# Kernel optimization log

Measured on AMD Instinct MI355X. Metric: run time of the kernel, lower is better.

The kernel has to match this reference:

```python
import jax, jax.numpy as jnp
import numpy as np

# Constants (mirroring CONSTANTS.py choices)
BCL = 8          # BYTE_CONTEXT_LEN
BED = 32         # BYTE_EMBED_DIM
HID = 512        # CONVERSATIONAL_HIDDEN_DIM
VOCAB = 260      # BYTE_VOCAB_DIM
NULL = 256
SOS = 257
B, T = 64, 512
NUMD = 16
CTX_DIM = HID + (50 + 64 + 150) + NUMD  # 792
IN_DIM = CTX_DIM + BCL * BED            # 1048


def setup_inputs() -> dict:
    key = jax.random.key(0)
    ks = jax.random.split(key, 20)
    s = 0.05
    return {
        "embedded_conversation_context": jax.random.normal(ks[0], (B, HID), jnp.float32),
        "next_packet_categorical": jax.random.randint(ks[1], (B, 3), 0, 10),
        "next_packet_numerical": jax.random.normal(ks[2], (B, NUMD), jnp.float32),
        "target_payload": jax.random.randint(ks[3], (B, T), 0, 256),
        "cat_emb_0": jax.random.normal(ks[4], (10, 50), jnp.float32) * s,
        "cat_emb_1": jax.random.normal(ks[5], (128, 64), jnp.float32) * s,
        "cat_emb_2": jax.random.normal(ks[6], (300, 150), jnp.float32) * s,
        "byte_emb": jax.random.normal(ks[7], (VOCAB, BED), jnp.float32) * s,
        "W_ih0": jax.random.normal(ks[8], (4 * HID, IN_DIM), jnp.float32) * s,
        "W_hh0": jax.random.normal(ks[9], (4 * HID, HID), jnp.float32) * s,
        "b_ih0": jax.random.normal(ks[10], (4 * HID,), jnp.float32) * s,
        "b_hh0": jax.random.normal(ks[11], (4 * HID,), jnp.float32) * s,
        "W_ih1": jax.random.normal(ks[12], (4 * HID, HID), jnp.float32) * s,
        "W_hh1": jax.random.normal(ks[13], (4 * HID, HID), jnp.float32) * s,
        "b_ih1": jax.random.normal(ks[14], (4 * HID,), jnp.float32) * s,
        "b_hh1": jax.random.normal(ks[15], (4 * HID,), jnp.float32) * s,
        "W_out": jax.random.normal(ks[16], (VOCAB - 4, HID), jnp.float32) * s,
        "b_out": jax.random.normal(ks[17], (VOCAB - 4,), jnp.float32) * s,
    }


def _lstm_layer(x, W_ih, W_hh, b_ih, b_hh):
    # x: [B, T, D] -> outputs [B, T, H]; torch gate order i, f, g, o
    xt = jnp.swapaxes(x, 0, 1)  # [T, B, D]
    gx = jnp.einsum('tbd,gd->tbg', xt, W_ih) + b_ih  # precompute input gates
    h0 = jnp.zeros((x.shape[0], HID), x.dtype)
    c0 = jnp.zeros((x.shape[0], HID), x.dtype)

    def step(carry, g_in):
        h, c = carry
        g = g_in + h @ W_hh.T + b_hh
        i, f, gg, o = jnp.split(g, 4, axis=-1)
        c = jax.nn.sigmoid(f) * c + jax.nn.sigmoid(i) * jnp.tanh(gg)
        h = jax.nn.sigmoid(o) * jnp.tanh(c)
        return (h, c), h

    _, ys = jax.lax.scan(step, (h0, c0), gx)
    return jnp.swapaxes(ys, 0, 1)  # [B, T, H]


def reference(embedded_conversation_context, next_packet_categorical,
              next_packet_numerical, target_payload,
              cat_emb_0, cat_emb_1, cat_emb_2, byte_emb,
              W_ih0, W_hh0, b_ih0, b_hh0,
              W_ih1, W_hh1, b_ih1, b_hh1,
              W_out, b_out):
    # categorical embeddings + context concat
    cat = jnp.concatenate([
        cat_emb_0[next_packet_categorical[:, 0]],
        cat_emb_1[next_packet_categorical[:, 1]],
        cat_emb_2[next_packet_categorical[:, 2]],
    ], axis=-1)
    context = jnp.concatenate([embedded_conversation_context, cat,
                               next_packet_numerical], axis=-1)  # [B, CTX_DIM]

    # front-pad payload with NULL*(BCL-1) then SOS, embed, sliding windows
    bsz = target_payload.shape[0]
    padded = jnp.concatenate([
        jnp.full((bsz, BCL - 1), NULL, target_payload.dtype),
        jnp.full((bsz, 1), SOS, target_payload.dtype),
        target_payload,
    ], axis=1)                                     # [B, T+BCL]
    emb = byte_emb[padded]                          # [B, T+BCL, BED]
    idx = jnp.arange(T)[:, None] + jnp.arange(BCL)[None, :]  # [T, BCL]
    win = emb[:, idx].reshape(bsz, T, BCL * BED)    # fused sliding-window gather

    ctx_rep = jnp.broadcast_to(context[:, None, :], (bsz, T, context.shape[-1]))
    x = jnp.concatenate([ctx_rep, win], axis=-1)    # [B, T, IN_DIM]

    h1 = _lstm_layer(x, W_ih0, W_hh0, b_ih0, b_hh0)
    h2 = _lstm_layer(h1, W_ih1, W_hh1, b_ih1, b_hh1)
    logits = jnp.einsum('bth,vh->btv', h2, W_out) + b_out  # [B, T, 256]
    return logits
```

## Files before the change

### kernel.cpp

```cpp
#include <hip/hip_runtime.h>
#include <hip/hip_bf16.h>
#include <math.h>

typedef __bf16 bf16;
typedef __bf16 bf16x8 __attribute__((ext_vector_type(8)));
typedef float  f32x4  __attribute__((ext_vector_type(4)));
typedef unsigned long long u64;

#define MFMA16(a, b, c) __builtin_amdgcn_mfma_f32_16x16x32_bf16((a), (b), (c), 0, 0, 0)

#define BB 64
#define TT 512
#define HH 512
#define G4 2048
#define NROW 32768
#define K2 1024
#define K3 1536
#define NWG 256
#define LROW 1032

#define AGLD(p) __hip_atomic_load((p), __ATOMIC_RELAXED, __HIP_MEMORY_SCOPE_AGENT)
#define AGST(p, v) __hip_atomic_store((p), (v), __ATOMIC_RELAXED, __HIP_MEMORY_SCOPE_AGENT)

__device__ __forceinline__ float sigmoidf_(float x) { return 1.0f / (1.0f + expf(-x)); }

__device__ __forceinline__ unsigned pack32(float h) {
    bf16 hh = (bf16)h;
    bf16 hl = (bf16)(h - (float)hh);
    unsigned short uh = __builtin_bit_cast(unsigned short, hh);
    unsigned short ul = __builtin_bit_cast(unsigned short, hl);
    return (unsigned)uh | ((unsigned)ul << 16);
}

__global__ void pad_bytes(const int* __restrict__ payload, int* __restrict__ bytes) {
    int b = blockIdx.x;
    for (int p = threadIdx.x; p < 520; p += blockDim.x)
        bytes[b * 520 + p] = (p < 7) ? 256 : ((p == 7) ? 257 : payload[b * 512 + p - 8]);
}

__global__ void build_Z(const float* __restrict__ Wih0, const float* __restrict__ bemb,
                        float* __restrict__ Z) {
    int v = blockIdx.x, j = blockIdx.y;
    __shared__ float e[32];
    if (threadIdx.x < 32) e[threadIdx.x] = bemb[v * 32 + threadIdx.x];
    __syncthreads();
#pragma unroll
    for (int i = 0; i < 8; i++) {
        int mp = threadIdx.x + i * 256;
        int u = mp >> 2, g = mp & 3;
        const float* wr = Wih0 + (size_t)(g * 512 + u) * 1048 + 792 + j * 32;
        float sum = 0.f;
#pragma unroll
        for (int kk = 0; kk < 32; kk++) sum += wr[kk] * e[kk];
        Z[((size_t)(v * 8 + j)) * G4 + mp] = sum;
    }
}

__global__ void build_ctxg(const float* __restrict__ ecc, const int* __restrict__ npc,
                           const float* __restrict__ npn,
                           const float* __restrict__ cat0, const float* __restrict__ cat1,
                           const float* __restrict__ cat2,
                           const float* __restrict__ bih0, const float* __restrict__ bhh0,
                           const float* __restrict__ Wih0, float* __restrict__ ctxg) {
    int b = blockIdx.x;
    __shared__ float cs[792];
    for (int k = threadIdx.x; k < 792; k += blockDim.x) {
        float v;
        if (k < 512)       v = ecc[b * 512 + k];
        else if (k < 562)  v = cat0[npc[b * 3 + 0] * 50 + (k - 512)];
        else if (k < 626)  v = cat1[npc[b * 3 + 1] * 64 + (k - 562)];
        else if (k < 776)  v = cat2[npc[b * 3 + 2] * 150 + (k - 626)];
        else               v = npn[b * 16 + (k - 776)];
        cs[k] = v;
    }
    __syncthreads();
#pragma unroll
    for (int i = 0; i < 8; i++) {
        int mp = threadIdx.x + i * 256;
        int u = mp >> 2, g = mp & 3;
        int orow = g * 512 + u;
        const float* wr = Wih0 + (size_t)orow * 1048;
        float sum = bih0[orow] + bhh0[orow];
        for (int k = 0; k < 792; k++) sum += wr[k] * cs[k];
        ctxg[b * G4 + mp] = sum;
    }
}

__global__ void conv_w0(const float* __restrict__ Whh0, bf16* __restrict__ W0p) {
    int rp = blockIdx.x; int u = rp >> 2, g = rp & 3;
    const float* src = Whh0 + (size_t)(g * 512 + u) * 512;
    bf16* dst = W0p + (size_t)rp * K2;
    for (int k = threadIdx.x; k < 512; k += blockDim.x) {
        float w = src[k]; bf16 hi = (bf16)w; bf16 lo = (bf16)(w - (float)hi);
        dst[k] = hi; dst[512 + k] = lo;
    }
}
__global__ void conv_w1(const float* __restrict__ Wih1, const float* __restrict__ Whh1,
                        bf16* __restrict__ W1p) {
    int rp = blockIdx.x; int u = rp >> 2, g = rp & 3;
    const float* s0 = Wih1 + (size_t)(g * 512 + u) * 512;
    const float* s1 = Whh1 + (size_t)(g * 512 + u) * 512;
    bf16* dst = W1p + (size_t)rp * (2 * K2);
    for (int k = threadIdx.x; k < 512; k += blockDim.x) {
        float w0 = s0[k]; bf16 h0 = (bf16)w0; bf16 l0 = (bf16)(w0 - (float)h0);
        dst[k] = h0; dst[512 + k] = l0;
        float w1 = s1[k]; bf16 h1 = (bf16)w1; bf16 l1 = (bf16)(w1 - (float)h1);
        dst[1024 + k] = h1; dst[1536 + k] = l1;
    }
}
__global__ void conv_wout(const float* __restrict__ Wout, bf16* __restrict__ Woutp) {
    int r = blockIdx.x;
    const float* src = Wout + (size_t)r * 512;
    bf16* dst = Woutp + (size_t)r * K3;
    for (int k = threadIdx.x; k < 512; k += blockDim.x) {
        float w = src[k]; bf16 hi = (bf16)w; bf16 lo = (bf16)(w - (float)hi);
        dst[k] = hi; dst[512 + k] = hi; dst[1024 + k] = lo;
    }
}
__global__ void conv_bias(const float* __restrict__ bih1, const float* __restrict__ bhh1,
                          float* __restrict__ bias1p) {
    int rp = blockIdx.x * blockDim.x + threadIdx.x;
    if (rp >= G4) return;
    int u = rp >> 2, g = rp & 3; int orow = g * 512 + u;
    bias1p[rp] = bih1[orow] + bhh1[orow];
}

__device__ __forceinline__ void group_barrier(unsigned* slots, int myslot, int bg,
                                              int tid, unsigned s1) {
    __syncthreads();
    __threadfence_block();
    if (tid == 0) AGST(&slots[myslot], s1);
    if (tid < 64) {
        int p = tid;
        int wpoll = (p < 32) ? (p * 4 + bg) : (128 + (p - 32) * 4 + bg);
        while (AGLD(&slots[wpoll]) < s1) __builtin_amdgcn_s_sleep(1);
    }
    __threadfence_block();
    __syncthreads();
}

__global__ __launch_bounds__(256, 1) void lstm_persist(
        const bf16* __restrict__ W0p, const bf16* __restrict__ W1p,
        const float* __restrict__ bias1p, const float* __restrict__ ctxg,
        const float* __restrict__ Z, const int* __restrict__ bytes,
        bf16* __restrict__ h0a, bf16* __restrict__ h0b,
        bf16* __restrict__ h1a, bf16* __restrict__ h1b,
        bf16* __restrict__ h2all, unsigned* __restrict__ slots) {
    __shared__ __align__(16) bf16 lds[2][16][LROW];
    int w = blockIdx.x, tid = threadIdx.x;
    int wave = tid >> 6, lane = tid & 63, l15 = lane & 15, q = lane >> 4;

    if (w < 128) {
        int mg = w >> 2, bg = w & 3;
        int b = bg * 16 + l15;
        int u = mg * 16 + wave * 4 + q;
        int u0 = mg * 16 + wave * 4;
        bf16x8 A[16][2];
        {
            const bf16* Ab = W0p + (size_t)(mg * 64 + wave * 16 + l15) * K2 + q * 8;
#pragma unroll
            for (int ks = 0; ks < 16; ks++) {
                A[ks][0] = *(const bf16x8*)(Ab + ks * 32);
                A[ks][1] = *(const bf16x8*)(Ab + 512 + ks * 32);
            }
        }
        f32x4 ctxgv = *(const f32x4*)&ctxg[b * G4 + 4 * u];
        const int* bp0 = bytes + b * 520;
        float c = 0.f;
        for (int s = 0; s <= TT; s++) {
            if (s < TT) {
                int t = s;
                const bf16* hr = (s & 1) ? h0a : h0b;
                const u64* g64 = (const u64*)(hr + (size_t)(bg * 16) * K2);
                u64 tmp[16];
#pragma unroll
                for (int i = 0; i < 8; i++) {
                    int cch = tid + i * 256;
                    tmp[2 * i]     = AGLD(&g64[2 * cch]);
                    tmp[2 * i + 1] = AGLD(&g64[2 * cch + 1]);
                }
                int vt[8];
#pragma unroll
                for (int j = 0; j < 8; j++) vt[j] = bp0[t + j];
                f32x4 g = ctxgv;
#pragma unroll
                for (int j = 0; j < 8; j++)
                    g += *(const f32x4*)&Z[((size_t)((vt[j] << 3) + j)) * G4 + 4 * u];
#pragma unroll
                for (int i = 0; i < 8; i++) {
                    int cch = tid + i * 256;
                    int br = cch >> 7, off = cch & 127;
                    u64 pr[2] = { tmp[2 * i], tmp[2 * i + 1] };
                    *(int4*)&lds[0][br][off * 8] = *(const int4*)pr;
                }
                __syncthreads();
                f32x4 a0 = {0.f,0.f,0.f,0.f}, a1 = a0, a2 = a0;
#pragma unroll
                for (int ks = 0; ks < 16; ks++) {
                    bf16x8 bhh = *(const bf16x8*)&lds[0][l15][ks * 32 + q * 8];
                    bf16x8 bhl = *(const bf16x8*)&lds[0][l15][512 + ks * 32 + q * 8];
                    a0 = MFMA16(A[ks][0], bhh, a0);
                    a1 = MFMA16(A[ks][0], bhl, a1);
                    a2 = MFMA16(A[ks][1], bhh, a2);
                }
                f32x4 acc = a0 + a1 + a2;
                float gi = acc[0] + g[0], gf = acc[1] + g[1], gg = acc[2] + g[2], go = acc[3] + g[3];
                float cnew = sigmoidf_(gf) * c + sigmoidf_(gi) * tanhf(gg);
                c = cnew;
                float h = sigmoidf_(go) * tanhf(cnew);
                unsigned hv = pack32(h);
                unsigned p0 = __shfl(hv, l15);
                unsigned p1 = __shfl(hv, l15 + 16);
                unsigned p2 = __shfl(hv, l15 + 32);
                unsigned p3 = __shfl(hv, l15 + 48);
                if (q == 0) {
                    u64 hhp = (u64)(p0 & 0xFFFFu) | ((u64)(p1 & 0xFFFFu) << 16)
                            | ((u64)(p2 & 0xFFFFu) << 32) | ((u64)(p3 & 0xFFFFu) << 48);
                    u64 hlp = (u64)(p0 >> 16) | ((u64)(p1 >> 16) << 16)
                            | ((u64)(p2 >> 16) << 32) | ((u64)(p3 >> 16) << 48);
                    bf16* hw = ((s & 1) ? h0b : h0a) + (size_t)b * K2;
                    AGST((u64*)&hw[u0], hhp);
                    AGST((u64*)&hw[512 + u0], hlp);
                }
            }
            if (s < TT) group_barrier(slots, w, bg, tid, (unsigned)(s + 1));
        }
    } else {
        int v = w - 128;
        int mg = v >> 2, bg = v & 3;
        int b = bg * 16 + l15;
        int u = mg * 16 + wave * 4 + q;
        int u0 = mg * 16 + wave * 4;
        bf16x8 A[2][16][2];
        {
            const bf16* Ab = W1p + (size_t)(mg * 64 + wave * 16 + l15) * (2 * K2) + q * 8;
#pragma unroll
            for (int m = 0; m < 2; m++)
#pragma unroll
                for (int ks = 0; ks < 16; ks++) {
                    A[m][ks][0] = *(const bf16x8*)(Ab + m * 1024 + ks * 32);
                    A[m][ks][1] = *(const bf16x8*)(Ab + m * 1024 + 512 + ks * 32);
                }
        }
        f32x4 bi = *(const f32x4*)&bias1p[4 * u];
        float c = 0.f;
        for (int s = 0; s <= TT; s++) {
            if (s >= 1) {
                int t = s - 1;
                const bf16* hr0 = (s & 1) ? h0a : h0b;
                const bf16* hr1 = (s & 1) ? h1a : h1b;
                const u64* g0 = (const u64*)(hr0 + (size_t)(bg * 16) * K2);
                const u64* g1 = (const u64*)(hr1 + (size_t)(bg * 16) * K2);
                u64 tmp[32];
#pragma unroll
                for (int i = 0; i < 8; i++) {
                    int cch = tid + i * 256;
                    tmp[2 * i]      = AGLD(&g0[2 * cch]);
                    tmp[2 * i + 1]  = AGLD(&g0[2 * cch + 1]);
                    tmp[16 + 2 * i] = AGLD(&g1[2 * cch]);
                    tmp[17 + 2 * i] = AGLD(&g1[2 * cch + 1]);
                }
#pragma unroll
                for (int i = 0; i < 8; i++) {
                    int cch = tid + i * 256;
                    int br = cch >> 7, off = cch & 127;
                    u64 p0_[2] = { tmp[2 * i], tmp[2 * i + 1] };
                    u64 p1_[2] = { tmp[16 + 2 * i], tmp[17 + 2 * i] };
                    *(int4*)&lds[0][br][off * 8] = *(const int4*)p0_;
                    *(int4*)&lds[1][br][off * 8] = *(const int4*)p1_;
                }
                __syncthreads();
                f32x4 a0 = {0.f,0.f,0.f,0.f}, a1 = a0, a2 = a0;
#pragma unroll
                for (int ks = 0; ks < 16; ks++) {
                    bf16x8 b0h = *(const bf16x8*)&lds[0][l15][ks * 32 + q * 8];
                    bf16x8 b0l = *(const bf16x8*)&lds[0][l15][512 + ks * 32 + q * 8];
                    a0 = MFMA16(A[0][ks][0], b0h, a0);
                    a1 = MFMA16(A[0][ks][0], b0l, a1);
                    a2 = MFMA16(A[0][ks][1], b0h, a2);
                    bf16x8 b1h = *(const bf16x8*)&lds[1][l15][ks * 32 + q * 8];
                    bf16x8 b1l = *(const bf16x8*)&lds[1][l15][512 + ks * 32 + q * 8];
                    a0 = MFMA16(A[1][ks][0], b1h, a0);
                    a1 = MFMA16(A[1][ks][0], b1l, a1);
                    a2 = MFMA16(A[1][ks][1], b1h, a2);
                }
                f32x4 acc = a0 + a1 + a2;
                float gi = acc[0] + bi[0], gf = acc[1] + bi[1], gg = acc[2] + bi[2], go = acc[3] + bi[3];
                float cnew = sigmoidf_(gf) * c + sigmoidf_(gi) * tanhf(gg);
                c = cnew;
                float h = sigmoidf_(go) * tanhf(cnew);
                unsigned hv = pack32(h);
                unsigned p0 = __shfl(hv, l15);
                unsigned p1 = __shfl(hv, l15 + 16);
                unsigned p2 = __shfl(hv, l15 + 32);
                unsigned p3 = __shfl(hv, l15 + 48);
                if (q == 0) {
                    u64 hhp = (u64)(p0 & 0xFFFFu) | ((u64)(p1 & 0xFFFFu) << 16)
                            | ((u64)(p2 & 0xFFFFu) << 32) | ((u64)(p3 & 0xFFFFu) << 48);
                    u64 hlp = (u64)(p0 >> 16) | ((u64)(p1 >> 16) << 16)
                            | ((u64)(p2 >> 16) << 32) | ((u64)(p3 >> 16) << 48);
                    bf16* hw = ((s & 1) ? h1b : h1a) + (size_t)b * K2;
                    AGST((u64*)&hw[u0], hhp);
                    AGST((u64*)&hw[512 + u0], hlp);
                    bf16* h2 = h2all + ((size_t)(t * 64 + b)) * K2;
                    *(u64*)&h2[u0] = hhp;
                    *(u64*)&h2[512 + u0] = hlp;
                }
            }
            if (s < TT) group_barrier(slots, w, bg, tid, (unsigned)(s + 1));
        }
    }
}

__global__ __launch_bounds__(256, 2) void gemm_out(const bf16* __restrict__ Wp,
                                                   const bf16* __restrict__ H2,
                                                   const float* __restrict__ bout,
                                                   float* __restrict__ out) {
    __shared__ bf16 As[128 * 32];
    __shared__ bf16 Bs[128 * 32];
    int mt = blockIdx.x, nt = blockIdx.y;
    int tid = threadIdx.x, wave = tid >> 6, lane = tid & 63;
    int l15 = lane & 15, q = lane >> 4;
    int msub = (wave & 1) * 64, nsub = (wave >> 1) * 64;
    f32x4 acc[4][4] = {};
    const bf16* Abase = Wp + (size_t)(mt * 128) * K3;
    const bf16* Bbase = H2 + (size_t)(nt * 128) * K2;
    for (int ks = 0; ks < K3 / 32; ks++) {
        int k0 = ks * 32;
        int kb = (k0 < 1024) ? k0 : (k0 - 1024);
        __syncthreads();
#pragma unroll
        for (int rnd = 0; rnd < 2; rnd++) {
            int cch = tid + rnd * 256;
            int rr = cch >> 2, seg = cch & 3;
            *(int4*)&As[cch * 8] = *(const int4*)&Abase[(size_t)rr * K3 + k0 + seg * 8];
            *(int4*)&Bs[cch * 8] = *(const int4*)&Bbase[(size_t)rr * K2 + kb + seg * 8];
        }
        __syncthreads();
        bf16x8 af[4], bf_[4];
#pragma unroll
        for (int i = 0; i < 4; i++) af[i]  = *(const bf16x8*)&As[(msub + i * 16 + l15) * 32 + q * 8];
#pragma unroll
        for (int j = 0; j < 4; j++) bf_[j] = *(const bf16x8*)&Bs[(nsub + j * 16 + l15) * 32 + q * 8];
#pragma unroll
        for (int i = 0; i < 4; i++)
#pragma unroll
            for (int j = 0; j < 4; j++)
                acc[i][j] = MFMA16(af[i], bf_[j], acc[i][j]);
    }
#pragma unroll
    for (int i = 0; i < 4; i++) {
        int m = mt * 128 + msub + i * 16 + q * 4;
        f32x4 bi = *(const f32x4*)&bout[m];
#pragma unroll
        for (int j = 0; j < 4; j++) {
            int n = nt * 128 + nsub + j * 16 + l15;
            int t = n >> 6, b = n & 63;
            f32x4 v = acc[i][j] + bi;
            *(f32x4*)&out[((size_t)(b * 512 + t)) * 256 + m] = v;
        }
    }
}

extern "C" void kernel_launch(void* const* d_in, const int* in_sizes, int n_in,
                              void* d_out, int out_size, void* d_ws, size_t ws_size,
                              hipStream_t stream) {
    const float* ecc   = (const float*)d_in[0];
    const int*   npc   = (const int*)d_in[1];
    const float* npn   = (const float*)d_in[2];
    const int*   payld = (const int*)d_in[3];
    const float* cat0  = (const float*)d_in[4];
    const float* cat1  = (const float*)d_in[5];
    const float* cat2  = (const float*)d_in[6];
    const float* bemb  = (const float*)d_in[7];
    const float* Wih0  = (const float*)d_in[8];
    const float* Whh0  = (const float*)d_in[9];
    const float* bih0  = (const float*)d_in[10];
    const float* bhh0  = (const float*)d_in[11];
    const float* Wih1  = (const float*)d_in[12];
    const float* Whh1  = (const float*)d_in[13];
    const float* bih1  = (const float*)d_in[14];
    const float* bhh1  = (const float*)d_in[15];
    const float* Wout  = (const float*)d_in[16];
    const float* bout  = (const float*)d_in[17];
    float* out = (float*)d_out;

    char* ws = (char*)d_ws;
    size_t off = 0;
    auto alloc = [&](size_t bytes) -> void* {
        void* p = ws + off;
        off = (off + bytes + 255) & ~(size_t)255;
        return p;
    };

    size_t zoff = off;
    bf16* h0a = (bf16*)alloc((size_t)BB * K2 * 2);
    bf16* h0b = (bf16*)alloc((size_t)BB * K2 * 2);
    bf16* h1a = (bf16*)alloc((size_t)BB * K2 * 2);
    bf16* h1b = (bf16*)alloc((size_t)BB * K2 * 2);
    unsigned* slots = (unsigned*)alloc(NWG * 4);
    size_t zbytes = off - zoff;

    bf16* W0p    = (bf16*)alloc((size_t)G4 * K2 * 2);
    bf16* W1p    = (bf16*)alloc((size_t)G4 * 2 * K2 * 2);
    bf16* Woutp  = (bf16*)alloc((size_t)256 * K3 * 2);
    float* bias1p = (float*)alloc((size_t)G4 * 4);
    float* Z      = (float*)alloc((size_t)260 * 8 * G4 * 4);
    float* ctxg   = (float*)alloc((size_t)BB * G4 * 4);
    int*   bytesb = (int*)alloc((size_t)BB * 520 * 4);
    bf16* h2all   = (bf16*)alloc((size_t)NROW * K2 * 2);

    if (ws_size < off) return;

    hipMemsetAsync(ws + zoff, 0, zbytes, stream);

    pad_bytes <<<BB, 256, 0, stream>>>(payld, bytesb);
    build_Z   <<<dim3(260, 8), 256, 0, stream>>>(Wih0, bemb, Z);
    build_ctxg<<<BB, 256, 0, stream>>>(ecc, npc, npn, cat0, cat1, cat2, bih0, bhh0, Wih0, ctxg);
    conv_w0   <<<G4, 256, 0, stream>>>(Whh0, W0p);
    conv_w1   <<<G4, 256, 0, stream>>>(Wih1, Whh1, W1p);
    conv_wout <<<256, 256, 0, stream>>>(Wout, Woutp);
    conv_bias <<<8, 256, 0, stream>>>(bih1, bhh1, bias1p);

    lstm_persist<<<NWG, 256, 0, stream>>>(W0p, W1p, bias1p, ctxg, Z, bytesb,
                                          h0a, h0b, h1a, h1b, h2all, slots);

    gemm_out<<<dim3(2, 256), 256, 0, stream>>>(Woutp, h2all, bout, out);
}
```

Before: 4.597 ms.

## Halve persistent LSTM grid to 128 workgroups of 512 threads with buffer loads

Reorganizes the persistent LSTM kernel so each workgroup runs 8 waves covering 32 hidden units instead of 4 waves covering 16, halving the workgroup count and the number of slots each group barrier polls. It also changes the layout of the h exchange buffers to interleave hi/lo halves in 16-byte blocks, using raw buffer loads and stores with a cache-policy flag in place of relaxed agent-scope atomics. The LDS row padding is widened. Fewer participants per barrier should cut the cross-workgroup synchronisation cost per timestep. In exchange, each CU holds more waves, and the correctness of the buffer cache policy for coherent cross-CU communication is a risk.

Measured after the change: 4.649 ms. About the same (+1.1%).

```diff
diff --git a/kernel.cpp b/kernel.cpp
--- a/kernel.cpp
+++ b/kernel.cpp
@@ -5,7 +5,9 @@
 typedef __bf16 bf16;
 typedef __bf16 bf16x8 __attribute__((ext_vector_type(8)));
 typedef float  f32x4  __attribute__((ext_vector_type(4)));
+typedef int    i32x4  __attribute__((ext_vector_type(4)));
 typedef unsigned long long u64;
+typedef u64    u64x2  __attribute__((ext_vector_type(2)));
 
 #define MFMA16(a, b, c) __builtin_amdgcn_mfma_f32_16x16x32_bf16((a), (b), (c), 0, 0, 0)
 
@@ -17,10 +19,25 @@
 #define K2 1024
 #define K3 1536
 #define NWG 256
-#define LROW 1032
+#define LROW 1040
 
 #define AGLD(p) __hip_atomic_load((p), __ATOMIC_RELAXED, __HIP_MEMORY_SCOPE_AGENT)
 #define AGST(p, v) __hip_atomic_store((p), (v), __ATOMIC_RELAXED, __HIP_MEMORY_SCOPE_AGENT)
+
+__device__ f32x4 llvm_amdgcn_raw_buffer_load_v4f32(i32x4 srsrc, int voffset, int soffset,
+                                                   int cachepolicy) __asm("llvm.amdgcn.raw.buffer.load.v4f32");
+__device__ void llvm_amdgcn_raw_buffer_store_v4f32(f32x4 vdata, i32x4 srsrc, int voffset, int soffset,
+                                                   int cachepolicy) __asm("llvm.amdgcn.raw.buffer.store.v4f32");
+
+__device__ __forceinline__ i32x4 make_srd(const void* p) {
+    u64 a = (u64)p;
+    i32x4 r;
+    r.x = (int)(a & 0xffffffffu);
+    r.y = (int)(a >> 32);
+    r.z = -1;
+    r.w = 0x00020000;
+    return r;
+}
 
 __device__ __forceinline__ float sigmoidf_(float x) { return 1.0f / (1.0f + expf(-x)); }
 
@@ -130,16 +147,15 @@
     __syncthreads();
     __threadfence_block();
     if (tid == 0) AGST(&slots[myslot], s1);
-    if (tid < 64) {
-        int p = tid;
-        int wpoll = (p < 32) ? (p * 4 + bg) : (128 + (p - 32) * 4 + bg);
+    if (tid < 32) {
+        int wpoll = (tid < 16) ? (tid * 4 + bg) : (64 + (tid - 16) * 4 + bg);
         while (AGLD(&slots[wpoll]) < s1) __builtin_amdgcn_s_sleep(1);
     }
     __threadfence_block();
     __syncthreads();
 }
 
-__global__ __launch_bounds__(256, 1) void lstm_persist(
+__global__ __launch_bounds__(512, 1) void lstm_persist(
         const bf16* __restrict__ W0p, const bf16* __restrict__ W1p,
         const float* __restrict__ bias1p, const float* __restrict__ ctxg,
         const float* __restrict__ Z, const int* __restrict__ bytes,
@@ -148,16 +164,19 @@
         bf16* __restrict__ h2all, unsigned* __restrict__ slots) {
     __shared__ __align__(16) bf16 lds[2][16][LROW];
     int w = blockIdx.x, tid = threadIdx.x;
-    int wave = tid >> 6, lane = tid & 63, l15 = lane & 15, q = lane >> 4;
-
-    if (w < 128) {
+    int wv = tid >> 6, lane = tid & 63, l15 = lane & 15, q = lane >> 4;
+
+    i32x4 s_h0a = make_srd(h0a), s_h0b = make_srd(h0b);
+    i32x4 s_h1a = make_srd(h1a), s_h1b = make_srd(h1b);
+
+    if (w < 64) {
         int mg = w >> 2, bg = w & 3;
         int b = bg * 16 + l15;
-        int u = mg * 16 + wave * 4 + q;
-        int u0 = mg * 16 + wave * 4;
+        int u = mg * 32 + wv * 4 + q;
+        int blkid = mg * 8 + wv;
         bf16x8 A[16][2];
         {
-            const bf16* Ab = W0p + (size_t)(mg * 64 + wave * 16 + l15) * K2 + q * 8;
+            const bf16* Ab = W0p + (size_t)(mg * 128 + wv * 16 + l15) * K2 + q * 8;
 #pragma unroll
             for (int ks = 0; ks < 16; ks++) {
                 A[ks][0] = *(const bf16x8*)(Ab + ks * 32);
@@ -169,29 +188,28 @@
         float c = 0.f;
         for (int s = 0; s <= TT; s++) {
             if (s < TT) {
-                int t = s;
-                const bf16* hr = (s & 1) ? h0a : h0b;
-                const u64* g64 = (const u64*)(hr + (size_t)(bg * 16) * K2);
-                u64 tmp[16];
-#pragma unroll
-                for (int i = 0; i < 8; i++) {
-                    int cch = tid + i * 256;
-                    tmp[2 * i]     = AGLD(&g64[2 * cch]);
-                    tmp[2 * i + 1] = AGLD(&g64[2 * cch + 1]);
+                i32x4 srdr = (s & 1) ? s_h0a : s_h0b;
+                f32x4 t0[4];
+#pragma unroll
+                for (int i = 0; i < 4; i++) {
+                    int cch = tid + i * 512;
+                    int voff = (bg * 16 + (cch >> 7)) * 2048 + (cch & 127) * 16;
+                    t0[i] = llvm_amdgcn_raw_buffer_load_v4f32(srdr, voff, 0, 17);
                 }
                 int vt[8];
 #pragma unroll
-                for (int j = 0; j < 8; j++) vt[j] = bp0[t + j];
+                for (int j = 0; j < 8; j++) vt[j] = bp0[s + j];
                 f32x4 g = ctxgv;
 #pragma unroll
                 for (int j = 0; j < 8; j++)
                     g += *(const f32x4*)&Z[((size_t)((vt[j] << 3) + j)) * G4 + 4 * u];
 #pragma unroll
-                for (int i = 0; i < 8; i++) {
-                    int cch = tid + i * 256;
-                    int br = cch >> 7, off = cch & 127;
-                    u64 pr[2] = { tmp[2 * i], tmp[2 * i + 1] };
-                    *(int4*)&lds[0][br][off * 8] = *(const int4*)pr;
+                for (int i = 0; i < 4; i++) {
+                    int cch = tid + i * 512;
+                    int br = cch >> 7, blk = cch & 127;
+                    u64x2 pr = __builtin_bit_cast(u64x2, t0[i]);
+                    *(u64*)&lds[0][br][blk * 4]       = pr.x;
+                    *(u64*)&lds[0][br][512 + blk * 4] = pr.y;
                 }
                 __syncthreads();
                 f32x4 a0 = {0.f,0.f,0.f,0.f}, a1 = a0, a2 = a0;
@@ -214,26 +232,27 @@
                 unsigned p2 = __shfl(hv, l15 + 32);
                 unsigned p3 = __shfl(hv, l15 + 48);
                 if (q == 0) {
-                    u64 hhp = (u64)(p0 & 0xFFFFu) | ((u64)(p1 & 0xFFFFu) << 16)
-                            | ((u64)(p2 & 0xFFFFu) << 32) | ((u64)(p3 & 0xFFFFu) << 48);
-                    u64 hlp = (u64)(p0 >> 16) | ((u64)(p1 >> 16) << 16)
-                            | ((u64)(p2 >> 16) << 32) | ((u64)(p3 >> 16) << 48);
-                    bf16* hw = ((s & 1) ? h0b : h0a) + (size_t)b * K2;
-                    AGST((u64*)&hw[u0], hhp);
-                    AGST((u64*)&hw[512 + u0], hlp);
+                    i32x4 ov;
+                    ov.x = (int)((p0 & 0xffffu) | (p1 << 16));
+                    ov.y = (int)((p2 & 0xffffu) | (p3 << 16));
+                    ov.z = (int)((p0 >> 16) | (p1 & 0xffff0000u));
+                    ov.w = (int)((p2 >> 16) | (p3 & 0xffff0000u));
+                    llvm_amdgcn_raw_buffer_store_v4f32(__builtin_bit_cast(f32x4, ov),
+                        (s & 1) ? s_h0b : s_h0a, b * 2048 + blkid * 16, 0, 17);
                 }
             }
             if (s < TT) group_barrier(slots, w, bg, tid, (unsigned)(s + 1));
         }
     } else {
-        int v = w - 128;
+        int v = w - 64;
         int mg = v >> 2, bg = v & 3;
         int b = bg * 16 + l15;
-        int u = mg * 16 + wave * 4 + q;
-        int u0 = mg * 16 + wave * 4;
+        int u = mg * 32 + wv * 4 + q;
+        int u0 = mg * 32 + wv * 4;
+        int blkid = mg * 8 + wv;
         bf16x8 A[2][16][2];
         {
-            const bf16* Ab = W1p + (size_t)(mg * 64 + wave * 16 + l15) * (2 * K2) + q * 8;
+            const bf16* Ab = W1p + (size_t)(mg * 128 + wv * 16 + l15) * (2 * K2) + q * 8;
 #pragma unroll
             for (int m = 0; m < 2; m++)
 #pragma unroll
@@ -246,28 +265,26 @@
         float c = 0.f;
         for (int s = 0; s <= TT; s++) {
             if (s >= 1) {
-                int t = s - 1;
-                const bf16* hr0 = (s & 1) ? h0a : h0b;
-                const bf16* hr1 = (s & 1) ? h1a : h1b;
-                const u64* g0 = (const u64*)(hr0 + (size_t)(bg * 16) * K2);
-                const u64* g1 = (const u64*)(hr1 + (size_t)(bg * 16) * K2);
-                u64 tmp[32];
-#pragma unroll
-                for (int i = 0; i < 8; i++) {
-                    int cch = tid + i * 256;
-                    tmp[2 * i]      = AGLD(&g0[2 * cch]);
-                    tmp[2 * i + 1]  = AGLD(&g0[2 * cch + 1]);
-                    tmp[16 + 2 * i] = AGLD(&g1[2 * cch]);
-                    tmp[17 + 2 * i] = AGLD(&g1[2 * cch + 1]);
-                }
-#pragma unroll
-                for (int i = 0; i < 8; i++) {
-                    int cch = tid + i * 256;
-                    int br = cch >> 7, off = cch & 127;
-                    u64 p0_[2] = { tmp[2 * i], tmp[2 * i + 1] };
-                    u64 p1_[2] = { tmp[16 + 2 * i], tmp[17 + 2 * i] };
-                    *(int4*)&lds[0][br][off * 8] = *(const int4*)p0_;
-                    *(int4*)&lds[1][br][off * 8] = *(const int4*)p1_;
+                i32x4 srd0 = (s & 1) ? s_h0a : s_h0b;
+                i32x4 srd1 = (s & 1) ? s_h1a : s_h1b;
+                f32x4 t0[4], t1[4];
+#pragma unroll
+                for (int i = 0; i < 4; i++) {
+                    int cch = tid + i * 512;
+                    int voff = (bg * 16 + (cch >> 7)) * 2048 + (cch & 127) * 16;
+                    t0[i] = llvm_amdgcn_raw_buffer_load_v4f32(srd0, voff, 0, 17);
+                    t1[i] = llvm_amdgcn_raw_buffer_load_v4f32(srd1, voff, 0, 17);
+                }
+#pragma unroll
+                for (int i = 0; i < 4; i++) {
+                    int cch = tid + i * 512;
+                    int br = cch >> 7, blk = cch & 127;
+                    u64x2 pr0 = __builtin_bit_cast(u64x2, t0[i]);
+                    u64x2 pr1 = __builtin_bit_cast(u64x2, t1[i]);
+                    *(u64*)&lds[0][br][blk * 4]       = pr0.x;
+                    *(u64*)&lds[0][br][512 + blk * 4] = pr0.y;
+                    *(u64*)&lds[1][br][blk * 4]       = pr1.x;
+                    *(u64*)&lds[1][br][512 + blk * 4] = pr1.y;
                 }
                 __syncthreads();
                 f32x4 a0 = {0.f,0.f,0.f,0.f}, a1 = a0, a2 = a0;
@@ -295,14 +312,16 @@
                 unsigned p2 = __shfl(hv, l15 + 32);
                 unsigned p3 = __shfl(hv, l15 + 48);
                 if (q == 0) {
-                    u64 hhp = (u64)(p0 & 0xFFFFu) | ((u64)(p1 & 0xFFFFu) << 16)
-                            | ((u64)(p2 & 0xFFFFu) << 32) | ((u64)(p3 & 0xFFFFu) << 48);
-                    u64 hlp = (u64)(p0 >> 16) | ((u64)(p1 >> 16) << 16)
-                            | ((u64)(p2 >> 16) << 32) | ((u64)(p3 >> 16) << 48);
-                    bf16* hw = ((s & 1) ? h1b : h1a) + (size_t)b * K2;
-                    AGST((u64*)&hw[u0], hhp);
-                    AGST((u64*)&hw[512 + u0], hlp);
-                    bf16* h2 = h2all + ((size_t)(t * 64 + b)) * K2;
+                    i32x4 ov;
+                    ov.x = (int)((p0 & 0xffffu) | (p1 << 16));
+                    ov.y = (int)((p2 & 0xffffu) | (p3 << 16));
+                    ov.z = (int)((p0 >> 16) | (p1 & 0xffff0000u));
+                    ov.w = (int)((p2 >> 16) | (p3 & 0xffff0000u));
+                    llvm_amdgcn_raw_buffer_store_v4f32(__builtin_bit_cast(f32x4, ov),
+                        (s & 1) ? s_h1b : s_h1a, b * 2048 + blkid * 16, 0, 17);
+                    u64 hhp = ((u64)(unsigned)ov.y << 32) | (unsigned)ov.x;
+                    u64 hlp = ((u64)(unsigned)ov.w << 32) | (unsigned)ov.z;
+                    bf16* h2 = h2all + ((size_t)((s - 1) * 64 + b)) * K2;
                     *(u64*)&h2[u0] = hhp;
                     *(u64*)&h2[512 + u0] = hlp;
                 }
@@ -422,7 +441,7 @@
     conv_wout <<<256, 256, 0, stream>>>(Wout, Woutp);
     conv_bias <<<8, 256, 0, stream>>>(bih1, bhh1, bias1p);
 
-    lstm_persist<<<NWG, 256, 0, stream>>>(W0p, W1p, bias1p, ctxg, Z, bytesb,
+    lstm_persist<<<128, 512, 0, stream>>>(W0p, W1p, bias1p, ctxg, Z, bytesb,
                                           h0a, h0b, h1a, h1b, h2all, slots);
 
     gemm_out<<<dim3(2, 256), 256, 0, stream>>>(Woutp, h2all, bout, out);
```
